# Kernel tuning notes

Hardware: AMD Instinct MI355X
Metric: run time of the kernel (lower is better)

Reference implementation:

```python
import jax, jax.numpy as jnp
import numpy as np
import math

B, T, D, DA = 4, 4096, 1024, 64
N_LAYERS = 12  # scaling uses sqrt(DA) * 12 per the original module


def setup_inputs() -> dict:
    key = jax.random.key(0)
    ks = jax.random.split(key, 7)
    s = 1.0 / math.sqrt(D)
    return {
        "x": jax.random.normal(ks[0], (B, T, D), dtype=jnp.float32),
        "Wq": jax.random.normal(ks[1], (D, DA), dtype=jnp.float32) * s,
        "bq": jax.random.normal(ks[2], (DA,), dtype=jnp.float32) * 0.01,
        "Wk": jax.random.normal(ks[3], (D, DA), dtype=jnp.float32) * s,
        "bk": jax.random.normal(ks[4], (DA,), dtype=jnp.float32) * 0.01,
        "Wv": jax.random.normal(ks[5], (D, DA), dtype=jnp.float32) * s,
        "bv": jax.random.normal(ks[6], (DA,), dtype=jnp.float32) * 0.01,
    }


def reference(x, Wq, bq, Wk, bk, Wv, bv):
    # x: [B, T, D]
    q = jnp.einsum('btd,da->bta', x, Wq) + bq  # [B, T, DA]
    k = jnp.einsum('btd,da->bta', x, Wk) + bk
    v = jnp.einsum('btd,da->bta', x, Wv) + bv
    scale = 1.0 / (math.sqrt(DA) * N_LAYERS)
    scores = jnp.einsum('bqa,bka->bqk', q, k) * scale  # [B, T, T]
    causal = jnp.tril(jnp.ones((T, T), dtype=bool))
    scores = jnp.where(causal[None, :, :], scores, -jnp.inf)
    attn = jax.nn.softmax(scores, axis=-1)
    return jnp.einsum('bqk,bka->bqa', attn, v)  # [B, T, DA]
```

## Files before the change

### kernel.cpp

```cpp
#include <hip/hip_runtime.h>
#include <hip/hip_bf16.h>


#define T_SEQ 4096
#define NW 12

using bf16x8 = __bf16 __attribute__((ext_vector_type(8)));
using f32x16 = float __attribute__((ext_vector_type(16)));
using uint4v = unsigned int __attribute__((ext_vector_type(4)));

static constexpr float QSCALE = 1.4426950408889634f / 96.0f;

__device__ __forceinline__ unsigned short bf1(float v) {
    unsigned u = __builtin_bit_cast(unsigned, v);
    u += 0x7FFFu + ((u >> 16) & 1u);
    return (unsigned short)(u >> 16);
}
__device__ __forceinline__ unsigned cvt2(float lo, float hi) {
    unsigned r;
    asm("v_cvt_pk_bf16_f32 %0, %1, %2" : "=v"(r) : "v"(lo), "v"(hi));
    return r;
}
__device__ __forceinline__ void pswap(unsigned& a, unsigned& b) {
    asm volatile("v_permlane32_swap_b32 %0, %1" : "+v"(a), "+v"(b));
}
__device__ __forceinline__ float bflo(unsigned u) {
    return __builtin_bit_cast(float, u << 16);
}
__device__ __forceinline__ float bfhi(unsigned u) {
    return __builtin_bit_cast(float, u & 0xFFFF0000u);
}
__device__ __forceinline__ f32x16 zero16() {
    f32x16 z;
#pragma unroll
    for (int i = 0; i < 16; ++i) z[i] = 0.0f;
    return z;
}
#define MFMA32(a, b, c) __builtin_amdgcn_mfma_f32_32x32x16_bf16(a, b, c, 0, 0, 0)

__device__ __forceinline__ void gload_lds16(const float* g, float* l) {
    __builtin_amdgcn_global_load_lds(
        (const __attribute__((address_space(1))) float*)g,
        (__attribute__((address_space(3))) float*)l, 16, 0, 0);
}

__global__ __launch_bounds__(256) void prep_w(
        const float* __restrict__ Wq, const float* __restrict__ Wk,
        const float* __restrict__ Wv, const float* __restrict__ bq,
        const float* __restrict__ bk, const float* __restrict__ bv,
        unsigned short* __restrict__ Wt3, float* __restrict__ bias_t) {
    __shared__ float tile[64][65];
    const int tid = threadIdx.x;
    const int m = blockIdx.x >> 4, kt = blockIdx.x & 15, d0 = kt * 64;
    const float* W = (m == 0) ? Wq : (m == 1) ? Wk : Wv;
    const int a = tid & 63, r4 = tid >> 6;
#pragma unroll
    for (int j = 0; j < 16; ++j) {
        const int rr = r4 + 4 * j;
        tile[rr][a] = W[(size_t)(d0 + rr) * 64 + a];
    }
    __syncthreads();
    const float scl = (m == 0) ? QSCALE : 1.0f;
    const int dc = tid & 63, ar = tid >> 6;
#pragma unroll
    for (int j = 0; j < 16; ++j) {
        const int aa = ar + 4 * j;
        const int cg = m * 64 + aa;
        const size_t addr =
            ((size_t)(kt * 6 + (cg >> 5)) * 4 + (dc >> 4)) * 512 +
            ((cg & 31) + 32 * ((dc >> 3) & 1)) * 8 + (dc & 7);
        Wt3[addr] = bf1(tile[dc][aa] * scl);
    }
    if (kt == 0 && tid < 64) {
        const float* bb = (m == 0) ? bq : (m == 1) ? bk : bv;
        bias_t[m * 64 + tid] = bb[tid] * scl;
    }
}

__global__ __launch_bounds__(384, 3) void proj_kernel(
        const float* __restrict__ x, const unsigned short* __restrict__ Wt3,
        const float* __restrict__ bias_t, unsigned short* __restrict__ qs,
        unsigned short* __restrict__ ksf, unsigned short* __restrict__ vtf) {
    __shared__ float Ald[2][2048];

    const int tid = threadIdx.x;
    const int w = tid >> 6, l = tid & 63, g = l >> 5, c32 = l & 31;
    const int ct = w;
    const int rowbase = blockIdx.x * 32;

    const int j1 = w;
    const int row1 = 4 * j1 + (l >> 4);
    const float* gp1 = x + (size_t)(rowbase + row1) * 1024 +
                       (((l & 15) ^ (row1 & 7)) << 2);
    const bool has2 = (w < 2);
    const int j2 = 6 + w;
    const int row2 = 4 * j2 + (l >> 4);
    const float* gp2 = x + (size_t)(rowbase + row2) * 1024 +
                       (((l & 15) ^ (row2 & 7)) << 2);

    const unsigned short* Wb = Wt3 + (size_t)(ct * 4) * 512 + l * 8;

    f32x16 acc = zero16();

    gload_lds16(gp1, &Ald[0][j1 * 256]);
    if (has2) gload_lds16(gp2, &Ald[0][j2 * 256]);
    __syncthreads();

#pragma unroll
    for (int kt = 0; kt < 16; ++kt) {
        if (kt < 15) {
            gload_lds16(gp1 + (kt + 1) * 64, &Ald[(kt + 1) & 1][j1 * 256]);
            if (has2)
                gload_lds16(gp2 + (kt + 1) * 64, &Ald[(kt + 1) & 1][j2 * 256]);
        }
        const float* A = Ald[kt & 1];
        const unsigned short* Wkt = Wb + (size_t)kt * 12288;
#pragma unroll
        for (int kk = 0; kk < 4; ++kk) {
            const int blk = kk * 4 + g * 2;
            float4 f0 = *(const float4*)(A + c32 * 64 + ((blk ^ (c32 & 7)) << 2));
            float4 f1 = *(const float4*)(A + c32 * 64 + (((blk + 1) ^ (c32 & 7)) << 2));
            uint4v ua;
            ua[0] = cvt2(f0.x, f0.y); ua[1] = cvt2(f0.z, f0.w);
            ua[2] = cvt2(f1.x, f1.y); ua[3] = cvt2(f1.z, f1.w);
            bf16x8 af = __builtin_bit_cast(bf16x8, ua);
            bf16x8 bfr = *(const bf16x8*)(Wkt + kk * 512);
            acc = MFMA32(af, bfr, acc);
        }
        __syncthreads();
    }

    const int cg = ct * 32 + c32;
    const float bias = bias_t[cg];
    const int mat = cg >> 6, cm = cg & 63;
    if (mat == 2) {
#pragma unroll
        for (int q4 = 0; q4 < 4; ++q4) {
            const int rowg = rowbase + 8 * q4 + 4 * g;
            const int b = rowg >> 12, tl = rowg & (T_SEQ - 1);
            const int ch = tl >> 5;
            const int f = (cm >> 5) * 2 + (q4 >> 1);
            const int lane = (cm & 31) + 32 * (q4 & 1);
            unsigned lo = cvt2(acc[4 * q4 + 0] + bias, acc[4 * q4 + 1] + bias);
            unsigned hi = cvt2(acc[4 * q4 + 2] + bias, acc[4 * q4 + 3] + bias);
            *(uint2*)(vtf + ((size_t)b * 128 + ch) * 2048 + f * 512 +
                      lane * 8 + 4 * g) = make_uint2(lo, hi);
        }
    } else if (mat == 1) {
#pragma unroll
        for (int r = 0; r < 16; ++r) {
            const int rowg = rowbase + (r & 3) + 8 * (r >> 2) + 4 * g;
            const int b = rowg >> 12, tl = rowg & (T_SEQ - 1);
            ksf[((size_t)b * 128 + (tl >> 5)) * 2048 + (cm >> 4) * 512 +
                ((tl & 31) + 32 * ((cm >> 3) & 1)) * 8 + (cm & 7)] =
                bf1(acc[r] + bias);
        }
    } else {
#pragma unroll
        for (int r = 0; r < 16; ++r) {
            const int rowg = rowbase + (r & 3) + 8 * (r >> 2) + 4 * g;
            qs[(size_t)rowg * 64 + cm] = bf1(acc[r] + bias);
        }
    }
}

__global__ __launch_bounds__(768, 3) void attn_kernel(
        const unsigned short* __restrict__ qs, const unsigned short* __restrict__ ksf,
        const unsigned short* __restrict__ vtf, float* __restrict__ out) {
    __shared__ unsigned short Osh[NW][32][66];
    __shared__ float msh[NW][32];
    __shared__ float ssh[NW][32];

    const int tid = threadIdx.x;
    const int w = tid >> 6, l = tid & 63, g = l >> 5, c32 = l & 31;
    const int b = blockIdx.x & 3;
    const int pid = blockIdx.x >> 2;

    for (int tt = 0; tt < 2; ++tt) {
        const int jt = tt ? pid : 127 - pid;
        const int qbase = jt * 32;

        const unsigned short* qp =
            qs + ((size_t)b * T_SEQ + qbase + c32) * 64 + g * 8;
        bf16x8 qf[4];
#pragma unroll
        for (int t = 0; t < 4; ++t) qf[t] = *(const bf16x8*)(qp + 16 * t);

        const unsigned short* pKc = ksf + ((size_t)b * 128 + w) * 2048 + l * 8;
        const unsigned short* pVc = vtf + ((size_t)b * 128 + w) * 2048 + l * 8;

        auto loadK = [&](bf16x8(&kf)[4]) {
#pragma unroll
            for (int t = 0; t < 4; ++t)
                kf[t] = *(const bf16x8*)(pKc + t * 512);
            pKc += NW * 2048;
        };
        auto loadV = [&](bf16x8(&vf)[4]) {
#pragma unroll
            for (int f = 0; f < 4; ++f)
                vf[f] = *(const bf16x8*)(pVc + f * 512);
            pVc += NW * 2048;
        };

        const int nch = (jt >= w) ? (jt - w) / NW + 1 : 0;
        const bool hasDiag = (jt >= w) && ((jt - w) % NW == 0);
        float m = -INFINITY, ssum = 0.0f;
        f32x16 o0 = zero16(), o1 = zero16();
        f32x16 s_cur;
        bf16x8 k0[4], k1[4], vR[4];

        if (nch > 0) {
            loadK(k0);
            f32x16 t = zero16();
#pragma unroll
            for (int t4 = 0; t4 < 4; ++t4) t = MFMA32(k0[t4], qf[t4], t);
            s_cur = t;
        }

        auto STEP = [&](bf16x8(&kn)[4], int i) {
            loadV(vR);
            if (i + 1 < nch) loadK(kn);
            if (hasDiag && i == nch - 1) {
#pragma unroll
                for (int r = 0; r < 16; ++r) {
                    const int kl = (r & 3) + 8 * (r >> 2) + 4 * g;
                    if (kl > c32) s_cur[r] = -1e30f;
                }
            }
            float a0 = fmaxf(fmaxf(s_cur[0], s_cur[1]), fmaxf(s_cur[2], s_cur[3]));
            float a1 = fmaxf(fmaxf(s_cur[4], s_cur[5]), fmaxf(s_cur[6], s_cur[7]));
            float a2 = fmaxf(fmaxf(s_cur[8], s_cur[9]), fmaxf(s_cur[10], s_cur[11]));
            float a3 = fmaxf(fmaxf(s_cur[12], s_cur[13]), fmaxf(s_cur[14], s_cur[15]));
            float pm = fmaxf(fmaxf(a0, a1), fmaxf(a2, a3));
            if (!__all(pm <= m + 8.0f)) {
                float rmax = fmaxf(pm, __shfl_xor(pm, 32, 64));
                const float mn = fmaxf(m, rmax);
                const float alpha = exp2f(m - mn);
#pragma unroll
                for (int r = 0; r < 16; ++r) { o0[r] *= alpha; o1[r] *= alpha; }
                ssum *= alpha;
                m = mn;
            }
            float p[16];
#pragma unroll
            for (int r = 0; r < 16; ++r) p[r] = exp2f(s_cur[r] - m);
            float s0 = (p[0] + p[1]) + (p[2] + p[3]);
            float s1 = (p[4] + p[5]) + (p[6] + p[7]);
            float s2 = (p[8] + p[9]) + (p[10] + p[11]);
            float s3 = (p[12] + p[13]) + (p[14] + p[15]);
            ssum += (s0 + s1) + (s2 + s3);
            unsigned c01 = cvt2(p[0], p[1]), c23 = cvt2(p[2], p[3]);
            unsigned c45 = cvt2(p[4], p[5]), c67 = cvt2(p[6], p[7]);
            pswap(c01, c45); pswap(c23, c67);
            unsigned c89 = cvt2(p[8], p[9]), cab = cvt2(p[10], p[11]);
            unsigned ccd = cvt2(p[12], p[13]), cef = cvt2(p[14], p[15]);
            pswap(c89, ccd); pswap(cab, cef);
            uint4v u0; u0[0] = c01; u0[1] = c23; u0[2] = c45; u0[3] = c67;
            uint4v u1; u1[0] = c89; u1[1] = cab; u1[2] = ccd; u1[3] = cef;
            bf16x8 pb0 = __builtin_bit_cast(bf16x8, u0);
            bf16x8 pb1 = __builtin_bit_cast(bf16x8, u1);
            __builtin_amdgcn_s_setprio(1);
            o0 = MFMA32(vR[0], pb0, o0);
            o0 = MFMA32(vR[1], pb1, o0);
            o1 = MFMA32(vR[2], pb0, o1);
            o1 = MFMA32(vR[3], pb1, o1);
            if (i + 1 < nch) {
                f32x16 t = zero16();
#pragma unroll
                for (int t4 = 0; t4 < 4; ++t4) t = MFMA32(kn[t4], qf[t4], t);
                s_cur = t;
            }
            __builtin_amdgcn_s_setprio(0);
        };

        int i = 0;
        while (i < nch) {
            STEP(k1, i); ++i;
            if (i < nch) { STEP(k0, i); ++i; }
        }
        ssum += __shfl_xor(ssum, 32, 64);

        if (l < 32) { msh[w][l] = m; ssh[w][l] = ssum; }
#pragma unroll
        for (int q4 = 0; q4 < 4; ++q4) {
            const int base = 8 * q4 + 4 * g;
            *(unsigned*)&Osh[w][c32][base]      = cvt2(o0[4 * q4], o0[4 * q4 + 1]);
            *(unsigned*)&Osh[w][c32][base + 2]  = cvt2(o0[4 * q4 + 2], o0[4 * q4 + 3]);
            *(unsigned*)&Osh[w][c32][base + 32] = cvt2(o1[4 * q4], o1[4 * q4 + 1]);
            *(unsigned*)&Osh[w][c32][base + 34] = cvt2(o1[4 * q4 + 2], o1[4 * q4 + 3]);
        }
        __syncthreads();

        if (tid < 512) {
            const int qrow = tid >> 4, e4 = tid & 15;
            float M = -INFINITY;
            float mw[NW];
#pragma unroll
            for (int u = 0; u < NW; ++u) { mw[u] = msh[u][qrow]; M = fmaxf(M, mw[u]); }
            float den = 0.0f;
            float r0 = 0.f, r1 = 0.f, r2 = 0.f, r3 = 0.f;
#pragma unroll
            for (int u = 0; u < NW; ++u) {
                const float scu = exp2f(mw[u] - M);
                den += ssh[u][qrow] * scu;
                const unsigned ua = *(const unsigned*)&Osh[u][qrow][4 * e4];
                const unsigned ub = *(const unsigned*)&Osh[u][qrow][4 * e4 + 2];
                r0 += bflo(ua) * scu;
                r1 += bfhi(ua) * scu;
                r2 += bflo(ub) * scu;
                r3 += bfhi(ub) * scu;
            }
            const float inv = 1.0f / den;
            float4 st;
            st.x = r0 * inv; st.y = r1 * inv; st.z = r2 * inv; st.w = r3 * inv;
            *(float4*)(out + ((size_t)b * T_SEQ + qbase + qrow) * 64 + 4 * e4) = st;
        }
        __syncthreads();
    }
}

extern "C" void kernel_launch(void* const* d_in, const int* in_sizes, int n_in,
                              void* d_out, int out_size, void* d_ws, size_t ws_size,
                              hipStream_t stream) {
    const float* x  = (const float*)d_in[0];
    const float* Wq = (const float*)d_in[1];
    const float* bq = (const float*)d_in[2];
    const float* Wk = (const float*)d_in[3];
    const float* bk = (const float*)d_in[4];
    const float* Wv = (const float*)d_in[5];
    const float* bv = (const float*)d_in[6];
    float* out = (float*)d_out;

    char* ws = (char*)d_ws;
    unsigned short* Wt3    = (unsigned short*)(ws);
    float*          bias_t = (float*)(ws + 393216);
    unsigned short* qsb    = (unsigned short*)(ws + (1u << 20));
    unsigned short* ksb    = (unsigned short*)(ws + (3u << 20));
    unsigned short* vtb    = (unsigned short*)(ws + (5u << 20));

    prep_w<<<48, 256, 0, stream>>>(Wq, Wk, Wv, bq, bk, bv, Wt3, bias_t);
    proj_kernel<<<512, 384, 0, stream>>>(x, Wt3, bias_t, qsb, ksb, vtb);
    attn_kernel<<<256, 768, 0, stream>>>(qsb, ksb, vtb, out);
}
```

Measured before the change: 50.17 us.

## Triple-buffer x tiles and register-prefetch weights in projection GEMM loop

The projection kernel moves from a double-buffered to a triple-buffered LDS staging of x, issuing loads two k-tiles ahead. Weight fragments are prefetched one stage ahead into ping-pong register arrays. The full __syncthreads is replaced by hand-counted s_waitcnt vmcnt plus s_barrier, so outstanding global loads no longer have to drain each iteration. This raises LDS usage to 24KB per block, which may affect occupancy, and relies on exact vmcnt counts being correct.

```diff
diff --git a/kernel.cpp b/kernel.cpp
--- a/kernel.cpp
+++ b/kernel.cpp
@@ -81,7 +81,7 @@
         const float* __restrict__ x, const unsigned short* __restrict__ Wt3,
         const float* __restrict__ bias_t, unsigned short* __restrict__ qs,
         unsigned short* __restrict__ ksf, unsigned short* __restrict__ vtf) {
-    __shared__ float Ald[2][2048];
+    __shared__ float Ald[3][2048];
 
     const int tid = threadIdx.x;
     const int w = tid >> 6, l = tid & 63, g = l >> 5, c32 = l & 31;
@@ -101,20 +101,31 @@
     const unsigned short* Wb = Wt3 + (size_t)(ct * 4) * 512 + l * 8;
 
     f32x16 acc = zero16();
+    bf16x8 bA[4], bB[4];
 
     gload_lds16(gp1, &Ald[0][j1 * 256]);
     if (has2) gload_lds16(gp2, &Ald[0][j2 * 256]);
-    __syncthreads();
-
-#pragma unroll
-    for (int kt = 0; kt < 16; ++kt) {
+    gload_lds16(gp1 + 64, &Ald[1][j1 * 256]);
+    if (has2) gload_lds16(gp2 + 64, &Ald[1][j2 * 256]);
+#pragma unroll
+    for (int f = 0; f < 4; ++f) bA[f] = *(const bf16x8*)(Wb + f * 512);
+    if (has2) asm volatile("s_waitcnt vmcnt(6)" ::: "memory");
+    else      asm volatile("s_waitcnt vmcnt(5)" ::: "memory");
+    __builtin_amdgcn_s_barrier();
+    __builtin_amdgcn_sched_barrier(0);
+
+    auto STAGE = [&](bf16x8(&bc)[4], bf16x8(&bn)[4], int kt) {
         if (kt < 15) {
-            gload_lds16(gp1 + (kt + 1) * 64, &Ald[(kt + 1) & 1][j1 * 256]);
+            const unsigned short* Wn = Wb + (size_t)(kt + 1) * 12288;
+#pragma unroll
+            for (int f = 0; f < 4; ++f) bn[f] = *(const bf16x8*)(Wn + f * 512);
+        }
+        if (kt < 14) {
+            gload_lds16(gp1 + (kt + 2) * 64, &Ald[(kt + 2) % 3][j1 * 256]);
             if (has2)
-                gload_lds16(gp2 + (kt + 1) * 64, &Ald[(kt + 1) & 1][j2 * 256]);
-        }
-        const float* A = Ald[kt & 1];
-        const unsigned short* Wkt = Wb + (size_t)kt * 12288;
+                gload_lds16(gp2 + (kt + 2) * 64, &Ald[(kt + 2) % 3][j2 * 256]);
+        }
+        const float* A = Ald[kt % 3];
 #pragma unroll
         for (int kk = 0; kk < 4; ++kk) {
             const int blk = kk * 4 + g * 2;
@@ -124,10 +135,24 @@
             ua[0] = cvt2(f0.x, f0.y); ua[1] = cvt2(f0.z, f0.w);
             ua[2] = cvt2(f1.x, f1.y); ua[3] = cvt2(f1.z, f1.w);
             bf16x8 af = __builtin_bit_cast(bf16x8, ua);
-            bf16x8 bfr = *(const bf16x8*)(Wkt + kk * 512);
-            acc = MFMA32(af, bfr, acc);
-        }
-        __syncthreads();
+            acc = MFMA32(af, bc[kk], acc);
+        }
+        if (kt < 14) {
+            if (has2) asm volatile("s_waitcnt vmcnt(6) lgkmcnt(0)" ::: "memory");
+            else      asm volatile("s_waitcnt vmcnt(5) lgkmcnt(0)" ::: "memory");
+            __builtin_amdgcn_s_barrier();
+            __builtin_amdgcn_sched_barrier(0);
+        } else if (kt == 14) {
+            asm volatile("s_waitcnt vmcnt(4) lgkmcnt(0)" ::: "memory");
+            __builtin_amdgcn_s_barrier();
+            __builtin_amdgcn_sched_barrier(0);
+        }
+    };
+
+#pragma unroll
+    for (int kt = 0; kt < 16; kt += 2) {
+        STAGE(bA, bB, kt);
+        STAGE(bB, bA, kt + 1);
     }
 
     const int cg = ct * 32 + c32;
```

Measured after the change: 49.16 us. 1.02x faster.

## Restructure projection kernel with split-K warps, triple-buffered LDS and register-prefetched weights

Applied to the files above, without the earlier changes.

Projection warps now split the K dimension in two halves, each computing two 32-column tiles (one full Q/K/V matrix per warp pair), with a final LDS reduction across the halves. Input x is staged in 128-column chunks through a three-deep LDS ring with explicit vmcnt waits, and weight fragments are double-buffered in registers, loaded one stage ahead. The aim is fewer barriers and better overlap of global loads with MFMA work, at the cost of more registers, a larger LDS footprint and an extra cross-warp reduction step.

```diff
diff --git a/kernel.cpp b/kernel.cpp
--- a/kernel.cpp
+++ b/kernel.cpp
@@ -81,85 +81,155 @@
         const float* __restrict__ x, const unsigned short* __restrict__ Wt3,
         const float* __restrict__ bias_t, unsigned short* __restrict__ qs,
         unsigned short* __restrict__ ksf, unsigned short* __restrict__ vtf) {
-    __shared__ float Ald[2][2048];
+    __shared__ float Ald[3 * 4096];
 
     const int tid = threadIdx.x;
     const int w = tid >> 6, l = tid & 63, g = l >> 5, c32 = l & 31;
-    const int ct = w;
+    const int kh = w & 1, cn = w >> 1;
     const int rowbase = blockIdx.x * 32;
 
-    const int j1 = w;
-    const int row1 = 4 * j1 + (l >> 4);
-    const float* gp1 = x + (size_t)(rowbase + row1) * 1024 +
-                       (((l & 15) ^ (row1 & 7)) << 2);
-    const bool has2 = (w < 2);
-    const int j2 = 6 + w;
-    const int row2 = 4 * j2 + (l >> 4);
-    const float* gp2 = x + (size_t)(rowbase + row2) * 1024 +
-                       (((l & 15) ^ (row2 & 7)) << 2);
-
-    const unsigned short* Wb = Wt3 + (size_t)(ct * 4) * 512 + l * 8;
-
-    f32x16 acc = zero16();
-
-    gload_lds16(gp1, &Ald[0][j1 * 256]);
-    if (has2) gload_lds16(gp2, &Ald[0][j2 * 256]);
-    __syncthreads();
-
-#pragma unroll
-    for (int kt = 0; kt < 16; ++kt) {
-        if (kt < 15) {
-            gload_lds16(gp1 + (kt + 1) * 64, &Ald[(kt + 1) & 1][j1 * 256]);
-            if (has2)
-                gload_lds16(gp2 + (kt + 1) * 64, &Ald[(kt + 1) & 1][j2 * 256]);
-        }
-        const float* A = Ald[kt & 1];
-        const unsigned short* Wkt = Wb + (size_t)kt * 12288;
+    const int j0 = w, j1 = w + 6, j2 = w + 12;
+    const bool has3 = (w < 4);
+    auto gsrc = [&](int j) {
+        const int row = 2 * j + (l >> 5);
+        const int fp = (((l & 31) ^ (row & 7)) << 2);
+        return x + (size_t)(rowbase + row) * 1024 +
+               (fp < 64 ? fp : 512 + fp - 64);
+    };
+    const float* gp0 = gsrc(j0);
+    const float* gp1 = gsrc(j1);
+    const float* gp2 = has3 ? gsrc(j2) : gp0;
+
+    const unsigned short* WbL = Wt3 + l * 8;
+    const int sz = c32 & 7;
+
+    f32x16 acc0 = zero16(), acc1 = zero16();
+    bf16x8 bA[8], bB[8];
+
+    auto loadB = [&](bf16x8(&bn)[8], int s) {
+        const int kt = kh * 8 + s;
+#pragma unroll
+        for (int sub = 0; sub < 2; ++sub) {
+            const int ct = 2 * cn + sub;
+#pragma unroll
+            for (int kk = 0; kk < 4; ++kk)
+                bn[sub * 4 + kk] =
+                    *(const bf16x8*)(WbL + (size_t)((kt * 6 + ct) * 4 + kk) * 512);
+        }
+    };
+    auto dmaStage = [&](int s) {
+        float* base = Ald + (s % 3) * 4096;
+        gload_lds16(gp0 + s * 64, base + j0 * 256);
+        gload_lds16(gp1 + s * 64, base + j1 * 256);
+        if (has3) gload_lds16(gp2 + s * 64, base + j2 * 256);
+    };
+
+    loadB(bA, 0);
+    dmaStage(0);
+    dmaStage(1);
+    if (has3) asm volatile("s_waitcnt vmcnt(3)" ::: "memory");
+    else      asm volatile("s_waitcnt vmcnt(2)" ::: "memory");
+    __builtin_amdgcn_s_barrier();
+    __builtin_amdgcn_sched_barrier(0);
+
+    auto STAGE = [&](bf16x8(&bc)[8], bf16x8(&bn)[8], int s) {
+        if (s < 7) loadB(bn, s + 1);
+        if (s < 6) dmaStage(s + 2);
+        const float* A = Ald + (s % 3) * 4096;
 #pragma unroll
         for (int kk = 0; kk < 4; ++kk) {
-            const int blk = kk * 4 + g * 2;
-            float4 f0 = *(const float4*)(A + c32 * 64 + ((blk ^ (c32 & 7)) << 2));
-            float4 f1 = *(const float4*)(A + c32 * 64 + (((blk + 1) ^ (c32 & 7)) << 2));
+            const int Bw = kh * 16 + kk * 4 + g * 2;
+            float4 f0 = *(const float4*)(A + c32 * 128 + ((Bw ^ sz) << 2));
+            float4 f1 = *(const float4*)(A + c32 * 128 + (((Bw + 1) ^ sz) << 2));
             uint4v ua;
             ua[0] = cvt2(f0.x, f0.y); ua[1] = cvt2(f0.z, f0.w);
             ua[2] = cvt2(f1.x, f1.y); ua[3] = cvt2(f1.z, f1.w);
             bf16x8 af = __builtin_bit_cast(bf16x8, ua);
-            bf16x8 bfr = *(const bf16x8*)(Wkt + kk * 512);
-            acc = MFMA32(af, bfr, acc);
-        }
-        __syncthreads();
-    }
-
-    const int cg = ct * 32 + c32;
-    const float bias = bias_t[cg];
-    const int mat = cg >> 6, cm = cg & 63;
-    if (mat == 2) {
+            acc0 = MFMA32(af, bc[kk], acc0);
+            acc1 = MFMA32(af, bc[4 + kk], acc1);
+        }
+        if (s < 6) {
+            if (has3) asm volatile("s_waitcnt vmcnt(11) lgkmcnt(0)" ::: "memory");
+            else      asm volatile("s_waitcnt vmcnt(10) lgkmcnt(0)" ::: "memory");
+            __builtin_amdgcn_s_barrier();
+            __builtin_amdgcn_sched_barrier(0);
+        } else if (s == 6) {
+            asm volatile("s_waitcnt vmcnt(8) lgkmcnt(0)" ::: "memory");
+            __builtin_amdgcn_s_barrier();
+            __builtin_amdgcn_sched_barrier(0);
+        }
+    };
+
+#pragma unroll
+    for (int s = 0; s < 8; s += 2) {
+        STAGE(bA, bB, s);
+        STAGE(bB, bA, s + 1);
+    }
+
+    asm volatile("s_waitcnt lgkmcnt(0)" ::: "memory");
+    __builtin_amdgcn_s_barrier();
+    float* Osum = Ald;
+    if (kh == 1) {
+        float* o = Osum + ((size_t)cn * 64 + l) * 32;
+#pragma unroll
+        for (int r = 0; r < 16; r += 4) {
+            *(float4*)(o + r) = make_float4(acc0[r], acc0[r + 1], acc0[r + 2], acc0[r + 3]);
+            *(float4*)(o + 16 + r) = make_float4(acc1[r], acc1[r + 1], acc1[r + 2], acc1[r + 3]);
+        }
+    }
+    __syncthreads();
+    if (kh == 1) return;
+    {
+        const float* o = Osum + ((size_t)cn * 64 + l) * 32;
+#pragma unroll
+        for (int r = 0; r < 16; r += 4) {
+            float4 a = *(const float4*)(o + r);
+            float4 b4 = *(const float4*)(o + 16 + r);
+            acc0[r] += a.x; acc0[r + 1] += a.y; acc0[r + 2] += a.z; acc0[r + 3] += a.w;
+            acc1[r] += b4.x; acc1[r + 1] += b4.y; acc1[r + 2] += b4.z; acc1[r + 3] += b4.w;
+        }
+    }
+
+    const float bias0 = bias_t[cn * 64 + c32];
+    const float bias1 = bias_t[cn * 64 + 32 + c32];
+    if (cn == 2) {
 #pragma unroll
         for (int q4 = 0; q4 < 4; ++q4) {
             const int rowg = rowbase + 8 * q4 + 4 * g;
             const int b = rowg >> 12, tl = rowg & (T_SEQ - 1);
             const int ch = tl >> 5;
-            const int f = (cm >> 5) * 2 + (q4 >> 1);
-            const int lane = (cm & 31) + 32 * (q4 & 1);
-            unsigned lo = cvt2(acc[4 * q4 + 0] + bias, acc[4 * q4 + 1] + bias);
-            unsigned hi = cvt2(acc[4 * q4 + 2] + bias, acc[4 * q4 + 3] + bias);
-            *(uint2*)(vtf + ((size_t)b * 128 + ch) * 2048 + f * 512 +
-                      lane * 8 + 4 * g) = make_uint2(lo, hi);
-        }
-    } else if (mat == 1) {
+#pragma unroll
+            for (int sub = 0; sub < 2; ++sub) {
+                const f32x16& a = sub ? acc1 : acc0;
+                const float bias = sub ? bias1 : bias0;
+                const int cm = c32 + 32 * sub;
+                const int f = (cm >> 5) * 2 + (q4 >> 1);
+                const int lane = (cm & 31) + 32 * (q4 & 1);
+                unsigned lo = cvt2(a[4 * q4 + 0] + bias, a[4 * q4 + 1] + bias);
+                unsigned hi = cvt2(a[4 * q4 + 2] + bias, a[4 * q4 + 3] + bias);
+                *(uint2*)(vtf + ((size_t)b * 128 + ch) * 2048 + f * 512 +
+                          lane * 8 + 4 * g) = make_uint2(lo, hi);
+            }
+        }
+    } else if (cn == 1) {
 #pragma unroll
         for (int r = 0; r < 16; ++r) {
             const int rowg = rowbase + (r & 3) + 8 * (r >> 2) + 4 * g;
             const int b = rowg >> 12, tl = rowg & (T_SEQ - 1);
-            ksf[((size_t)b * 128 + (tl >> 5)) * 2048 + (cm >> 4) * 512 +
-                ((tl & 31) + 32 * ((cm >> 3) & 1)) * 8 + (cm & 7)] =
-                bf1(acc[r] + bias);
+#pragma unroll
+            for (int sub = 0; sub < 2; ++sub) {
+                const int cm = c32 + 32 * sub;
+                const float v = (sub ? acc1[r] : acc0[r]) + (sub ? bias1 : bias0);
+                ksf[((size_t)b * 128 + (tl >> 5)) * 2048 + (cm >> 4) * 512 +
+                    ((tl & 31) + 32 * ((cm >> 3) & 1)) * 8 + (cm & 7)] = bf1(v);
+            }
         }
     } else {
 #pragma unroll
         for (int r = 0; r < 16; ++r) {
             const int rowg = rowbase + (r & 3) + 8 * (r >> 2) + 4 * g;
-            qs[(size_t)rowg * 64 + cm] = bf1(acc[r] + bias);
+            qs[(size_t)rowg * 64 + c32] = bf1(acc0[r] + bias0);
+            qs[(size_t)rowg * 64 + 32 + c32] = bf1(acc1[r] + bias1);
         }
     }
 }
```

Measured after the change: 55.65 us. 10.9% more time.
